# Performance work log

Measured on AMD Instinct MI355X. Metric: run time of the kernel, lower is better.

Reference implementation:

```python
import jax, jax.numpy as jnp
import numpy as np

BONE_NUM = 16
THRESH = 0.7


def masked_l2(out, tar, mask):
    # out, tar: [B, C, H, W]; mask: [B, H, W]
    diff_norm = jnp.linalg.norm(out - tar, axis=1)          # [B, H, W]
    masked = jnp.where(mask > THRESH, diff_norm, 0.0)
    B = out.shape[0]
    flat_m = masked.reshape(B, -1)
    flat_d = diff_norm.reshape(B, -1)
    cnt = jnp.sum(flat_m != 0, axis=1)                       # device-side nonzero count
    per_sample = jnp.where(
        cnt > 0,
        flat_m.sum(axis=1) / jnp.maximum(cnt, 1).astype(flat_m.dtype),
        flat_d.mean(axis=1),
    )
    return per_sample.mean()


def pose_nocs_loss(pred_joint_map, pred_joint_score, out_mask, tar_joints):
    # pred_joint_map: [B, bn*3, H, W]; pred_joint_score: [B, bn, H, W]
    # out_mask: [B, H, W]; tar_joints: [B, bn, 3]
    B, _, H, W = pred_joint_map.shape
    bn = BONE_NUM
    jm = pred_joint_map.reshape(B, bn, 3, H, W) * out_mask[:, None, None]
    score = jax.nn.sigmoid(pred_joint_score) * out_mask[:, None]        # [B, bn, H, W]
    denom = score.reshape(B, bn, -1).sum(axis=2)[:, :, None, None] + 1e-5
    score_map = score / denom
    jm = jax.lax.stop_gradient(jm) * score_map[:, :, None]              # [B, bn, 3, H, W]
    pred_joint = jm.reshape(B, bn, 3, -1).sum(axis=3)                   # [B, bn, 3]
    loss = jnp.linalg.norm(pred_joint - tar_joints, axis=2).sum()
    return loss / (B * bn)


def setup_inputs() -> dict:
    key = jax.random.key(0)
    k1, k2, k3 = jax.random.split(key, 3)
    B, H, W = 4, 256, 256
    bn = BONE_NUM
    output = jax.random.normal(k1, (B, 4 + bn * 8 + 2, H, W), dtype=jnp.float32)
    tar_maps = jax.random.uniform(k2, (B, 4 + bn * 6 + 1, H, W), dtype=jnp.float32)
    tar_pose = jax.random.normal(k3, (B, bn, 6), dtype=jnp.float32)
    return {"output": output, "tar_maps": tar_maps, "tar_pose": tar_pose}


def reference(output, tar_maps, tar_pose):
    bn = BONE_NUM
    B = output.shape[0]

    # --- slice predictions ---
    pred_nocs = output[:, 0:3]
    mask_logits = output[:, 3]                                # sigmoid applied below
    pred_loc_map = jax.nn.sigmoid(output[:, 4:4 + bn * 3])
    pred_rot_map = jax.nn.sigmoid(output[:, 4 + bn * 3:4 + bn * 6])
    pred_skin_seg = output[:, 4 + bn * 6:4 + bn * 7 + 2]       # [B, bn+2, H, W]
    pred_joint_score = output[:, 4 + bn * 7 + 2:4 + bn * 8 + 2]  # [B, bn, H, W]

    # --- slice targets ---
    target_nocs = tar_maps[:, 0:3]
    target_mask = tar_maps[:, 3]
    tar_loc_map = jax.nn.sigmoid(tar_maps[:, 4:4 + bn * 3])
    tar_rot_map = jax.nn.sigmoid(tar_maps[:, 4 + bn * 3:4 + bn * 6])
    tar_skin_seg = tar_maps[:, 4 + bn * 6].astype(jnp.int32)   # [B, H, W]
    tar_loc = jax.nn.sigmoid(tar_pose[:, :, 0:3])
    tar_rot = jax.nn.sigmoid(tar_pose[:, :, 3:6])

    # --- BCE mask loss (on sigmoid(mask_logits) vs target_mask), stable form ---
    mask_loss = -jnp.mean(
        target_mask * jax.nn.log_sigmoid(mask_logits)
        + (1.0 - target_mask) * jax.nn.log_sigmoid(-mask_logits)
    )

    # --- masked L2 losses ---
    nocs_loss = masked_l2(pred_nocs, target_nocs, target_mask)
    loc_map_loss = masked_l2(pred_loc_map, tar_loc_map, target_mask)
    rot_map_loss = masked_l2(pred_rot_map, tar_rot_map, target_mask)

    # --- skinning cross entropy ---
    logits = jnp.transpose(pred_skin_seg, (0, 2, 3, 1)).reshape(-1, bn + 2)
    labels = tar_skin_seg.reshape(-1)
    logp = jax.nn.log_softmax(logits, axis=-1)
    skin_loss = -jnp.mean(jnp.take_along_axis(logp, labels[:, None], axis=1))

    # --- pose losses ---
    loc_loss = pose_nocs_loss(pred_loc_map, pred_joint_score, target_mask, tar_loc)
    rot_loss = pose_nocs_loss(pred_rot_map, pred_joint_score, target_mask, tar_rot)

    return jnp.stack([nocs_loss, mask_loss, loc_loss, loc_map_loss,
                      rot_loss, rot_map_loss, skin_loss])
```

## Files before the change

kernel.cpp:

```cpp
#include <hip/hip_runtime.h>
#include <math.h>

#define HW 65536
#define BN 16


__device__ __forceinline__ float fsig(float x) {
    return __builtin_amdgcn_rcpf(1.0f + __expf(-x));
}

__device__ __forceinline__ float wred(float v) {
#pragma unroll
    for (int off = 32; off; off >>= 1) v += __shfl_xor(v, off, 64);
    return v;
}

__global__ __launch_bounds__(256) void mvpm_main(const float* __restrict__ outp,
                                                 const float* __restrict__ tarp,
                                                 float* __restrict__ ws) {
    const int b = blockIdx.y;
    const int p = blockIdx.x * 256 + threadIdx.x;
    const float* ob = outp + (size_t)b * 134 * HW;
    const float* tb = tarp + (size_t)b * 101 * HW;
    const int lane = threadIdx.x & 63;
    const int wv = threadIdx.x >> 6;

    __shared__ float red[123][4];

#define STAGE(slot, val)                          \
    do {                                          \
        float _r = wred(val);                     \
        if (lane == 0) red[(slot)][wv] = _r;      \
    } while (0)

    const float m  = tb[3 * HW + p];
    const float mm = m * m;
    const bool sel = m > 0.7f;

    float dsq_loc = 0.0f, dsq_rot = 0.0f;
    for (int j = 0; j < BN; ++j) {
        float w = fsig(ob[(118 + j) * HW + p]) * m;
        STAGE(11 + j, w);
#pragma unroll
        for (int k = 0; k < 3; ++k) {
            const int c = 3 * j + k;
            float so = fsig(ob[(4 + c) * HW + p]);
            float st = fsig(tb[(4 + c) * HW + p]);
            float d  = so - st;
            dsq_loc += d * d;
            STAGE(27 + c, so * w * m);

            float so2 = fsig(ob[(52 + c) * HW + p]);
            float st2 = fsig(tb[(52 + c) * HW + p]);
            float d2  = so2 - st2;
            dsq_rot += d2 * d2;
            STAGE(75 + c, so2 * w * m);
        }
    }

    float d0 = ob[0 * HW + p] - tb[0 * HW + p];
    float d1 = ob[1 * HW + p] - tb[1 * HW + p];
    float d2n = ob[2 * HW + p] - tb[2 * HW + p];
    float dn = sqrtf(d0 * d0 + d1 * d1 + d2n * d2n);
    STAGE(2, sel ? dn : 0.0f);
    STAGE(3, (sel && dn != 0.0f) ? 1.0f : 0.0f);
    STAGE(4, dn);

    float dnl = sqrtf(dsq_loc);
    STAGE(5, sel ? dnl : 0.0f);
    STAGE(6, (sel && dnl != 0.0f) ? 1.0f : 0.0f);
    STAGE(7, dnl);

    float dnr = sqrtf(dsq_rot);
    STAGE(8, sel ? dnr : 0.0f);
    STAGE(9, (sel && dnr != 0.0f) ? 1.0f : 0.0f);
    STAGE(10, dnr);

    {
        float ml = ob[3 * HW + p];
        float t  = __logf(1.0f + __expf(-fabsf(ml)));
        float v  = m * fminf(ml, 0.0f) + (1.0f - m) * fminf(-ml, 0.0f) - t;
        STAGE(0, v);
    }

    {
        float x[18];
#pragma unroll
        for (int k = 0; k < 18; ++k) x[k] = ob[(100 + k) * HW + p];
        float mx = x[0];
#pragma unroll
        for (int k = 1; k < 18; ++k) mx = fmaxf(mx, x[k]);
        float se = 0.0f;
#pragma unroll
        for (int k = 0; k < 18; ++k) se += __expf(x[k] - mx);
        float lse = mx + __logf(se);
        int lab = (int)tb[100 * HW + p];
        lab = lab < 0 ? 0 : (lab > 17 ? 17 : lab);
        float xl = x[0];
#pragma unroll
        for (int k = 1; k < 18; ++k) xl = (lab == k) ? x[k] : xl;
        STAGE(1, lse - xl);
    }

    __syncthreads();
    if (threadIdx.x < 123) {
        float s = red[threadIdx.x][0] + red[threadIdx.x][1] +
                  red[threadIdx.x][2] + red[threadIdx.x][3];
        int g = (threadIdx.x < 2) ? threadIdx.x : (2 + b * 121 + (threadIdx.x - 2));
        atomicAdd(&ws[g], s);
    }
#undef STAGE
}

__global__ __launch_bounds__(64) void mvpm_fin(const float* __restrict__ ws,
                                               const float* __restrict__ tp,
                                               float* __restrict__ o) {
    const int t = threadIdx.x;
    const int b = t >> 4;
    const int j = t & 15;
    const int base = 2 + b * 121;

    float S = ws[base + 9 + j] + 1e-5f;
    float ln = 0.0f, rn = 0.0f;
#pragma unroll
    for (int c = 0; c < 3; ++c) {
        float pl = ws[base + 25 + 3 * j + c] / S;
        float tl = 1.0f / (1.0f + expf(-tp[t * 6 + c]));
        ln += (pl - tl) * (pl - tl);
        float pr = ws[base + 73 + 3 * j + c] / S;
        float tr = 1.0f / (1.0f + expf(-tp[t * 6 + 3 + c]));
        rn += (pr - tr) * (pr - tr);
    }
    ln = sqrtf(ln);
    rn = sqrtf(rn);
    float lsum = wred(ln);
    float rsum = wred(rn);

    if (t == 0) {
        float nocs = 0.0f, locm = 0.0f, rotm = 0.0f;
        for (int bb = 0; bb < 4; ++bb) {
            int ba = 2 + bb * 121;
            nocs += (ws[ba + 1] > 0.5f) ? ws[ba + 0] / ws[ba + 1] : ws[ba + 2] * (1.0f / HW);
            locm += (ws[ba + 4] > 0.5f) ? ws[ba + 3] / ws[ba + 4] : ws[ba + 5] * (1.0f / HW);
            rotm += (ws[ba + 7] > 0.5f) ? ws[ba + 6] / ws[ba + 7] : ws[ba + 8] * (1.0f / HW);
        }
        o[0] = nocs * 0.25f;
        o[1] = -ws[0] / (4.0f * HW);
        o[2] = lsum * (1.0f / 64.0f);
        o[3] = locm * 0.25f;
        o[4] = rsum * (1.0f / 64.0f);
        o[5] = rotm * 0.25f;
        o[6] = ws[1] / (4.0f * HW);
    }
}

extern "C" void kernel_launch(void* const* d_in, const int* in_sizes, int n_in,
                              void* d_out, int out_size, void* d_ws, size_t ws_size,
                              hipStream_t stream) {
    const float* outp = (const float*)d_in[0];
    const float* tarp = (const float*)d_in[1];
    const float* tpos = (const float*)d_in[2];
    float* o  = (float*)d_out;
    float* ws = (float*)d_ws;

    hipMemsetAsync(d_ws, 0, 486 * sizeof(float), stream);
    dim3 grid(HW / 256, 4);
    mvpm_main<<<grid, 256, 0, stream>>>(outp, tarp, ws);
    mvpm_fin<<<1, 64, 0, stream>>>(ws, tpos, o);
}
```

Baseline: 308.0 us.

## Split per-joint weighted sums into separate kernel with register accumulation

The single per-pixel kernel did 123 full wavefront shuffle reductions per block, one for each per-joint statistic. Those per-joint weighted sums now live in a second kernel, with one block per (batch, joint) slice. Each thread there accumulates over 16 pixels in registers and reduces only 7 values. The pixel kernel keeps the 11 global statistics and batches their shuffles. This removes most of the reduction and LDS traffic, at the cost of re-reading the loc/rot/score channels and recomputing their sigmoids in the second kernel.

```diff
diff --git a/kernel.cpp b/kernel.cpp
--- a/kernel.cpp
+++ b/kernel.cpp
@@ -15,9 +15,9 @@
     return v;
 }
 
-__global__ __launch_bounds__(256) void mvpm_main(const float* __restrict__ outp,
-                                                 const float* __restrict__ tarp,
-                                                 float* __restrict__ ws) {
+__global__ __launch_bounds__(256) void mvpm_pix(const float* __restrict__ outp,
+                                                const float* __restrict__ tarp,
+                                                float* __restrict__ ws) {
     const int b = blockIdx.y;
     const int p = blockIdx.x * 256 + threadIdx.x;
     const float* ob = outp + (size_t)b * 134 * HW;
@@ -25,109 +25,150 @@
     const int lane = threadIdx.x & 63;
     const int wv = threadIdx.x >> 6;
 
-    __shared__ float red[123][4];
-
-#define STAGE(slot, val)                          \
-    do {                                          \
-        float _r = wred(val);                     \
-        if (lane == 0) red[(slot)][wv] = _r;      \
-    } while (0)
-
-    const float m  = tb[3 * HW + p];
-    const float mm = m * m;
+    const float m = tb[3 * HW + p];
     const bool sel = m > 0.7f;
 
-    float dsq_loc = 0.0f, dsq_rot = 0.0f;
-    for (int j = 0; j < BN; ++j) {
-        float w = fsig(ob[(118 + j) * HW + p]) * m;
-        STAGE(11 + j, w);
-#pragma unroll
-        for (int k = 0; k < 3; ++k) {
-            const int c = 3 * j + k;
-            float so = fsig(ob[(4 + c) * HW + p]);
-            float st = fsig(tb[(4 + c) * HW + p]);
-            float d  = so - st;
-            dsq_loc += d * d;
-            STAGE(27 + c, so * w * m);
-
-            float so2 = fsig(ob[(52 + c) * HW + p]);
-            float st2 = fsig(tb[(52 + c) * HW + p]);
-            float d2  = so2 - st2;
-            dsq_rot += d2 * d2;
-            STAGE(75 + c, so2 * w * m);
-        }
-    }
+    const float ml = ob[3 * HW + p];
+    const float bce = m * fminf(ml, 0.0f) + (1.0f - m) * fminf(-ml, 0.0f)
+                      - __logf(1.0f + __expf(-fabsf(ml)));
 
     float d0 = ob[0 * HW + p] - tb[0 * HW + p];
     float d1 = ob[1 * HW + p] - tb[1 * HW + p];
-    float d2n = ob[2 * HW + p] - tb[2 * HW + p];
-    float dn = sqrtf(d0 * d0 + d1 * d1 + d2n * d2n);
-    STAGE(2, sel ? dn : 0.0f);
-    STAGE(3, (sel && dn != 0.0f) ? 1.0f : 0.0f);
-    STAGE(4, dn);
-
-    float dnl = sqrtf(dsq_loc);
-    STAGE(5, sel ? dnl : 0.0f);
-    STAGE(6, (sel && dnl != 0.0f) ? 1.0f : 0.0f);
-    STAGE(7, dnl);
-
-    float dnr = sqrtf(dsq_rot);
-    STAGE(8, sel ? dnr : 0.0f);
-    STAGE(9, (sel && dnr != 0.0f) ? 1.0f : 0.0f);
-    STAGE(10, dnr);
-
-    {
-        float ml = ob[3 * HW + p];
-        float t  = __logf(1.0f + __expf(-fabsf(ml)));
-        float v  = m * fminf(ml, 0.0f) + (1.0f - m) * fminf(-ml, 0.0f) - t;
-        STAGE(0, v);
-    }
-
-    {
-        float x[18];
-#pragma unroll
-        for (int k = 0; k < 18; ++k) x[k] = ob[(100 + k) * HW + p];
-        float mx = x[0];
-#pragma unroll
-        for (int k = 1; k < 18; ++k) mx = fmaxf(mx, x[k]);
-        float se = 0.0f;
-#pragma unroll
-        for (int k = 0; k < 18; ++k) se += __expf(x[k] - mx);
-        float lse = mx + __logf(se);
-        int lab = (int)tb[100 * HW + p];
-        lab = lab < 0 ? 0 : (lab > 17 ? 17 : lab);
-        float xl = x[0];
-#pragma unroll
-        for (int k = 1; k < 18; ++k) xl = (lab == k) ? x[k] : xl;
-        STAGE(1, lse - xl);
-    }
-
+    float d2 = ob[2 * HW + p] - tb[2 * HW + p];
+    const float dn = sqrtf(d0 * d0 + d1 * d1 + d2 * d2);
+
+    float dsl = 0.0f, dsr = 0.0f;
+#pragma unroll 4
+    for (int c = 0; c < 48; ++c) {
+        float so = fsig(ob[(4 + c) * HW + p]);
+        float st = fsig(tb[(4 + c) * HW + p]);
+        float d = so - st;
+        dsl += d * d;
+        float so2 = fsig(ob[(52 + c) * HW + p]);
+        float st2 = fsig(tb[(52 + c) * HW + p]);
+        float dd = so2 - st2;
+        dsr += dd * dd;
+    }
+    const float dnl = sqrtf(dsl);
+    const float dnr = sqrtf(dsr);
+
+    float x[18];
+#pragma unroll
+    for (int k = 0; k < 18; ++k) x[k] = ob[(100 + k) * HW + p];
+    float mx = x[0];
+#pragma unroll
+    for (int k = 1; k < 18; ++k) mx = fmaxf(mx, x[k]);
+    float se = 0.0f;
+#pragma unroll
+    for (int k = 0; k < 18; ++k) se += __expf(x[k] - mx);
+    float lse = mx + __logf(se);
+    int lab = (int)tb[100 * HW + p];
+    lab = lab < 0 ? 0 : (lab > 17 ? 17 : lab);
+    float xl = x[0];
+#pragma unroll
+    for (int k = 1; k < 18; ++k) xl = (lab == k) ? x[k] : xl;
+    const float skin = lse - xl;
+
+    float v[11];
+    v[0] = bce;
+    v[1] = skin;
+    v[2] = sel ? dn : 0.0f;
+    v[3] = (sel && dn != 0.0f) ? 1.0f : 0.0f;
+    v[4] = dn;
+    v[5] = sel ? dnl : 0.0f;
+    v[6] = (sel && dnl != 0.0f) ? 1.0f : 0.0f;
+    v[7] = dnl;
+    v[8] = sel ? dnr : 0.0f;
+    v[9] = (sel && dnr != 0.0f) ? 1.0f : 0.0f;
+    v[10] = dnr;
+
+#pragma unroll
+    for (int off = 32; off; off >>= 1) {
+#pragma unroll
+        for (int i = 0; i < 11; ++i) v[i] += __shfl_xor(v[i], off, 64);
+    }
+
+    __shared__ float red[11][4];
+    if (lane == 0) {
+#pragma unroll
+        for (int i = 0; i < 11; ++i) red[i][wv] = v[i];
+    }
     __syncthreads();
-    if (threadIdx.x < 123) {
+    if (threadIdx.x < 11) {
         float s = red[threadIdx.x][0] + red[threadIdx.x][1] +
                   red[threadIdx.x][2] + red[threadIdx.x][3];
-        int g = (threadIdx.x < 2) ? threadIdx.x : (2 + b * 121 + (threadIdx.x - 2));
+        int g = (threadIdx.x < 2) ? threadIdx.x : (2 + b * 9 + (threadIdx.x - 2));
         atomicAdd(&ws[g], s);
     }
-#undef STAGE
+}
+
+__global__ __launch_bounds__(256) void mvpm_joint(const float* __restrict__ outp,
+                                                  const float* __restrict__ tarp,
+                                                  float* __restrict__ ws) {
+    const int bj = blockIdx.y;
+    const int b = bj >> 4;
+    const int j = bj & 15;
+    const float* ob = outp + (size_t)b * 134 * HW;
+    const float* mp = tarp + (size_t)b * 101 * HW + 3 * HW;
+    const float* sp = ob + (118 + j) * HW;
+    const float* lp = ob + (4 + 3 * j) * HW;
+    const float* rp = ob + (52 + 3 * j) * HW;
+
+    const int base = blockIdx.x * 4096 + threadIdx.x;
+    const int lane = threadIdx.x & 63;
+    const int wv = threadIdx.x >> 6;
+
+    float S = 0.0f, nl0 = 0.0f, nl1 = 0.0f, nl2 = 0.0f,
+          nr0 = 0.0f, nr1 = 0.0f, nr2 = 0.0f;
+#pragma unroll 4
+    for (int i = 0; i < 16; ++i) {
+        const int p = base + i * 256;
+        const float m = mp[p];
+        const float w = fsig(sp[p]) * m;
+        S += w;
+        const float wm = w * m;
+        nl0 += fsig(lp[p]) * wm;
+        nl1 += fsig(lp[HW + p]) * wm;
+        nl2 += fsig(lp[2 * HW + p]) * wm;
+        nr0 += fsig(rp[p]) * wm;
+        nr1 += fsig(rp[HW + p]) * wm;
+        nr2 += fsig(rp[2 * HW + p]) * wm;
+    }
+
+    float v[7] = {S, nl0, nl1, nl2, nr0, nr1, nr2};
+#pragma unroll
+    for (int off = 32; off; off >>= 1) {
+#pragma unroll
+        for (int i = 0; i < 7; ++i) v[i] += __shfl_xor(v[i], off, 64);
+    }
+
+    __shared__ float red[7][4];
+    if (lane == 0) {
+#pragma unroll
+        for (int i = 0; i < 7; ++i) red[i][wv] = v[i];
+    }
+    __syncthreads();
+    if (threadIdx.x < 7) {
+        float s = red[threadIdx.x][0] + red[threadIdx.x][1] +
+                  red[threadIdx.x][2] + red[threadIdx.x][3];
+        atomicAdd(&ws[38 + bj * 7 + threadIdx.x], s);
+    }
 }
 
 __global__ __launch_bounds__(64) void mvpm_fin(const float* __restrict__ ws,
                                                const float* __restrict__ tp,
                                                float* __restrict__ o) {
     const int t = threadIdx.x;
-    const int b = t >> 4;
-    const int j = t & 15;
-    const int base = 2 + b * 121;
-
-    float S = ws[base + 9 + j] + 1e-5f;
+    const int base = 38 + t * 7;
+
+    float S = ws[base] + 1e-5f;
     float ln = 0.0f, rn = 0.0f;
 #pragma unroll
     for (int c = 0; c < 3; ++c) {
-        float pl = ws[base + 25 + 3 * j + c] / S;
+        float pl = ws[base + 1 + c] / S;
         float tl = 1.0f / (1.0f + expf(-tp[t * 6 + c]));
         ln += (pl - tl) * (pl - tl);
-        float pr = ws[base + 73 + 3 * j + c] / S;
+        float pr = ws[base + 4 + c] / S;
         float tr = 1.0f / (1.0f + expf(-tp[t * 6 + 3 + c]));
         rn += (pr - tr) * (pr - tr);
     }
@@ -139,7 +180,7 @@
     if (t == 0) {
         float nocs = 0.0f, locm = 0.0f, rotm = 0.0f;
         for (int bb = 0; bb < 4; ++bb) {
-            int ba = 2 + bb * 121;
+            int ba = 2 + bb * 9;
             nocs += (ws[ba + 1] > 0.5f) ? ws[ba + 0] / ws[ba + 1] : ws[ba + 2] * (1.0f / HW);
             locm += (ws[ba + 4] > 0.5f) ? ws[ba + 3] / ws[ba + 4] : ws[ba + 5] * (1.0f / HW);
             rotm += (ws[ba + 7] > 0.5f) ? ws[ba + 6] / ws[ba + 7] : ws[ba + 8] * (1.0f / HW);
@@ -164,7 +205,9 @@
     float* ws = (float*)d_ws;
 
     hipMemsetAsync(d_ws, 0, 486 * sizeof(float), stream);
-    dim3 grid(HW / 256, 4);
-    mvpm_main<<<grid, 256, 0, stream>>>(outp, tarp, ws);
+    dim3 gA(HW / 256, 4);
+    mvpm_pix<<<gA, 256, 0, stream>>>(outp, tarp, ws);
+    dim3 gB(16, 64);
+    mvpm_joint<<<gB, 256, 0, stream>>>(outp, tarp, ws);
     mvpm_fin<<<1, 64, 0, stream>>>(ws, tpos, o);
 }
```

New measurement: 294.3 us. 1.05x faster.
